# Performance work log

Hardware: AMD Instinct MI355X
Metric: run time of the kernel (lower is better)

## Reference

```python
import jax, jax.numpy as jnp
import numpy as np

EPSILON = 1e-8
DAMPING = 0.7
B, PREV, SIZE, NXT = 8192, 2000, 2000, 2000


def standardize(x):
    # per-sample standardization over features (torch.std uses ddof=1)
    mean = x.mean(axis=1, keepdims=True)
    std = jnp.std(x, axis=1, ddof=1, keepdims=True)
    return (x - mean) / (std + EPSILON)


def setup_inputs() -> dict:
    key = jax.random.key(0)
    ks = jax.random.split(key, 9)
    return {
        "prev_act": jax.random.normal(ks[0], (B, PREV), jnp.float32),
        "self_act": jax.random.normal(ks[1], (B, SIZE), jnp.float32),
        "next_act": jax.random.normal(ks[2], (B, NXT), jnp.float32),
        "forward_W": jax.random.normal(ks[3], (SIZE, PREV), jnp.float32) * 0.02,
        "forward_b": jax.random.normal(ks[4], (SIZE,), jnp.float32) * 0.02,
        "backward_W": jax.random.normal(ks[5], (SIZE, NXT), jnp.float32) * 0.02,
        "backward_b": jax.random.normal(ks[6], (SIZE,), jnp.float32) * 0.02,
        "lateral_W": jax.random.normal(ks[7], (SIZE, SIZE), jnp.float32) * 0.02,
        "lateral_b": jax.random.normal(ks[8], (SIZE,), jnp.float32) * 0.02,
    }


def reference(prev_act, self_act, next_act, forward_W, forward_b,
              backward_W, backward_b, lateral_W, lateral_b):
    # middle HiddenLayer forward: fwd(prev) + next.backward(next) + lateral(self)
    prev_s = standardize(prev_act)   # [B, PREV]
    next_s = standardize(next_act)   # [B, NXT]
    self_s = standardize(self_act)   # [B, SIZE]
    pre = (jnp.einsum('bp,sp->bs', prev_s, forward_W) + forward_b
           + jnp.einsum('bn,sn->bs', next_s, backward_W) + backward_b
           + jnp.einsum('bk,sk->bs', self_s, lateral_W) + lateral_b)
    new_act = jax.nn.relu(pre)
    # damped recurrent update
    return DAMPING * new_act + (1.0 - DAMPING) * self_act
```

## Files before the change

kernel.cpp:

```cpp
#include <hip/hip_runtime.h>
#include <hip/hip_bf16.h>

constexpr int BATCH = 8192;
constexpr int NREAL = 2000;
constexpr int KSLOT = 2048;
constexpr int KPAD  = 6144;
constexpr int NPAD  = 2048;
constexpr int NT    = KPAD / 64;

typedef short bf16x8 __attribute__((ext_vector_type(8)));
typedef float f32x4  __attribute__((ext_vector_type(4)));

__device__ inline void gload_lds16(const void* g, void* l) {
  __builtin_amdgcn_global_load_lds(
      (const __attribute__((address_space(1))) unsigned int*)g,
      (__attribute__((address_space(3))) unsigned int*)l,
      16, 0, 0);
}

__device__ inline unsigned short f2bf(float x) {
  union { float f; unsigned int u; } v;
  v.f = x;
  unsigned int r = v.u + 0x7fffu + ((v.u >> 16) & 1u);
  return (unsigned short)(r >> 16);
}

__global__ __launch_bounds__(256) void pack_kernel(
    const float* __restrict__ prev, const float* __restrict__ nxt,
    const float* __restrict__ selfa,
    const float* __restrict__ fW, const float* __restrict__ bW,
    const float* __restrict__ lW,
    unsigned short* __restrict__ Acat, unsigned short* __restrict__ Wcat) {
  const int mat = blockIdx.y;
  const int t = threadIdx.x;

  if (blockIdx.x >= BATCH) {
    const int s = blockIdx.x - BATCH;
    uint4 q = make_uint4(0, 0, 0, 0);
    if (s < NREAL && t < 250) {
      const float* src = ((mat == 0) ? fW : (mat == 1) ? bW : lW) +
                         (size_t)s * NREAL + t * 8;
      const float4* p = (const float4*)src;
      float4 a = p[0], b = p[1];
      q.x = (unsigned)f2bf(a.x) | ((unsigned)f2bf(a.y) << 16);
      q.y = (unsigned)f2bf(a.z) | ((unsigned)f2bf(a.w) << 16);
      q.z = (unsigned)f2bf(b.x) | ((unsigned)f2bf(b.y) << 16);
      q.w = (unsigned)f2bf(b.z) | ((unsigned)f2bf(b.w) << 16);
    }
    *(uint4*)(Wcat + (size_t)s * KPAD + mat * KSLOT + t * 8) = q;
    return;
  }

  __shared__ float red[4];
  const int row = blockIdx.x;
  const float* src = (mat == 0) ? prev : (mat == 1) ? nxt : selfa;

  float x[8];
  float s1 = 0.f;
  if (t < 250) {
    const float4* p = (const float4*)(src + (size_t)row * NREAL + t * 8);
    float4 a = p[0], b = p[1];
    x[0] = a.x; x[1] = a.y; x[2] = a.z; x[3] = a.w;
    x[4] = b.x; x[5] = b.y; x[6] = b.z; x[7] = b.w;
#pragma unroll
    for (int j = 0; j < 8; ++j) s1 += x[j];
  } else {
#pragma unroll
    for (int j = 0; j < 8; ++j) x[j] = 0.f;
  }
#pragma unroll
  for (int o = 32; o; o >>= 1) s1 += __shfl_xor(s1, o);
  if ((t & 63) == 0) red[t >> 6] = s1;
  __syncthreads();
  const float mean = (red[0] + red[1] + red[2] + red[3]) * (1.f / 2000.f);
  __syncthreads();

  float ss = 0.f;
  if (t < 250) {
#pragma unroll
    for (int j = 0; j < 8; ++j) { float d = x[j] - mean; ss += d * d; }
  }
#pragma unroll
  for (int o = 32; o; o >>= 1) ss += __shfl_xor(ss, o);
  if ((t & 63) == 0) red[t >> 6] = ss;
  __syncthreads();
  const float var = (red[0] + red[1] + red[2] + red[3]) * (1.f / 1999.f);
  const float scale = 1.f / (sqrtf(var) + 1e-8f);

  unsigned short o8[8];
  if (t < 250) {
#pragma unroll
    for (int j = 0; j < 8; ++j) o8[j] = f2bf((x[j] - mean) * scale);
  } else {
#pragma unroll
    for (int j = 0; j < 8; ++j) o8[j] = 0;
  }
  uint4 q;
  q.x = (unsigned)o8[0] | ((unsigned)o8[1] << 16);
  q.y = (unsigned)o8[2] | ((unsigned)o8[3] << 16);
  q.z = (unsigned)o8[4] | ((unsigned)o8[5] << 16);
  q.w = (unsigned)o8[6] | ((unsigned)o8[7] << 16);
  *(uint4*)(Acat + (size_t)row * KPAD + mat * KSLOT + t * 8) = q;
}

__global__ __launch_bounds__(512, 2) void gemm_kernel(
    const unsigned short* __restrict__ A,
    const unsigned short* __restrict__ W,
    const float* __restrict__ fb, const float* __restrict__ bb,
    const float* __restrict__ lb,
    const float* __restrict__ selfact,
    float* __restrict__ out) {
  __shared__ unsigned short lds[2][2][2][256][32];
  unsigned short* ldsF = &lds[0][0][0][0][0];

  const int tid  = threadIdx.x;
  const int wave = tid >> 6;
  const int lane = tid & 63;
  const int wm = wave >> 2;
  const int wn = wave & 3;

  const int nbid = (blockIdx.x & 7) * 32 + (blockIdx.x >> 3);
  const int bm = nbid >> 3;
  const int bn = nbid & 7;

  const int srow = tid >> 2;
  const int sc = (tid & 3) ^ ((srow >> 1) & 3);
  const unsigned short* Asrc =
      A + (size_t)(bm * 256 + srow) * KPAD + sc * 8;
  const unsigned short* Bsrc =
      W + (size_t)(bn * 256 + srow) * KPAD + sc * 8;

  const int pcx = (lane >> 4) ^ ((lane >> 1) & 3);
  const unsigned short* aF = ldsF + (wm * 128 + (lane & 15)) * 32 + pcx * 8;
  const unsigned short* bF = ldsF + (wn * 64 + (lane & 15)) * 32 + pcx * 8;

  f32x4 acc[8][4] = {};
  bf16x8 afA[4], afB[4], bf0[4], bf1[4];

#define STAGE(sb, mat, h, tt) { \
    const unsigned short* g_ = ((mat) ? Bsrc : Asrc) + (size_t)(tt) * 64 + (h) * 32; \
    unsigned short* d_ = ldsF + ((sb) * 4 + (mat) * 2 + (h)) * 8192 + wave * 64 * 8; \
    gload_lds16(g_, d_); \
    gload_lds16(g_ + (size_t)128 * KPAD, d_ + 512 * 8); \
  }

#define READ_AF(dst, bb, kk, mh) \
    _Pragma("unroll") for (int fm = 0; fm < 4; ++fm) \
      dst[fm] = *(const bf16x8*)(aF + ((bb) * 4 + (kk)) * 8192 + ((mh) * 64 + fm * 16) * 32);

#define READ_BF(dst, bb, kk) \
    _Pragma("unroll") for (int fn = 0; fn < 4; ++fn) \
      dst[fn] = *(const bf16x8*)(bF + ((bb) * 4 + 2 + (kk)) * 8192 + (fn * 16) * 32);

#define MFMA16(afr, bfr, mh) { \
    __builtin_amdgcn_s_setprio(1); \
    _Pragma("unroll") for (int fm = 0; fm < 4; ++fm) \
    _Pragma("unroll") for (int fn = 0; fn < 4; ++fn) \
      acc[(mh) * 4 + fm][fn] = __builtin_amdgcn_mfma_f32_16x16x32_bf16( \
          afr[fm], bfr[fn], acc[(mh) * 4 + fm][fn], 0, 0, 0); \
    __builtin_amdgcn_s_setprio(0); \
  }

  STAGE(0, 0, 0, 0)
  STAGE(0, 1, 0, 0)
  STAGE(0, 0, 1, 0)
  STAGE(0, 1, 1, 0)
  asm volatile("s_waitcnt vmcnt(4)" ::: "memory");
  __builtin_amdgcn_s_barrier();
  __builtin_amdgcn_sched_barrier(0);
  READ_AF(afA, 0, 0, 0)
  READ_BF(bf0, 0, 0)

  for (int t = 0; t < NT; ++t) {
    const int b = t & 1;
    const bool pf = (t + 1 < NT);
    __builtin_amdgcn_s_barrier();
    __builtin_amdgcn_sched_barrier(0);
    READ_AF(afB, b, 0, 1)
    if (pf) STAGE(b ^ 1, 0, 0, t + 1)
    MFMA16(afA, bf0, 0)
    asm volatile("s_waitcnt vmcnt(2)" ::: "memory");
    __builtin_amdgcn_s_barrier();
    __builtin_amdgcn_sched_barrier(0);
    READ_AF(afA, b, 1, 0)
    READ_BF(bf1, b, 1)
    if (pf) STAGE(b ^ 1, 1, 0, t + 1)
    MFMA16(afB, bf0, 1)
    __builtin_amdgcn_s_barrier();
    __builtin_amdgcn_sched_barrier(0);
    READ_AF(afB, b, 1, 1)
    if (pf) STAGE(b ^ 1, 0, 1, t + 1)
    MFMA16(afA, bf1, 0)
    asm volatile("s_waitcnt vmcnt(2)" ::: "memory");
    __builtin_amdgcn_s_barrier();
    __builtin_amdgcn_sched_barrier(0);
    if (pf) {
      READ_AF(afA, b ^ 1, 0, 0)
      READ_BF(bf0, b ^ 1, 0)
      STAGE(b ^ 1, 1, 1, t + 1)
    }
    MFMA16(afB, bf1, 1)
  }

  const int colLane = lane & 15;
  const int rowGrp  = (lane >> 4) * 4;
#pragma unroll
  for (int fn = 0; fn < 4; ++fn) {
    const int col = bn * 256 + wn * 64 + fn * 16 + colLane;
    if (col < NREAL) {
      const float bias = fb[col] + bb[col] + lb[col];
#pragma unroll
      for (int m = 0; m < 8; ++m) {
        const int row0 = bm * 256 + wm * 128 + m * 16 + rowGrp;
#pragma unroll
        for (int r = 0; r < 4; ++r) {
          const float pre = acc[m][fn][r] + bias;
          const size_t oi = (size_t)(row0 + r) * NREAL + col;
          out[oi] = 0.7f * fmaxf(pre, 0.f) + 0.3f * selfact[oi];
        }
      }
    }
  }
#undef MFMA16
#undef READ_BF
#undef READ_AF
#undef STAGE
}

extern "C" void kernel_launch(void* const* d_in, const int* in_sizes, int n_in,
                              void* d_out, int out_size, void* d_ws,
                              size_t ws_size, hipStream_t stream) {
  const float* prev = (const float*)d_in[0];
  const float* selfa = (const float*)d_in[1];
  const float* nxt  = (const float*)d_in[2];
  const float* fW = (const float*)d_in[3];
  const float* fb = (const float*)d_in[4];
  const float* bW = (const float*)d_in[5];
  const float* bb = (const float*)d_in[6];
  const float* lW = (const float*)d_in[7];
  const float* lb = (const float*)d_in[8];
  float* out = (float*)d_out;

  unsigned short* Acat = (unsigned short*)d_ws;
  unsigned short* Wcat = Acat + (size_t)BATCH * KPAD;

  pack_kernel<<<dim3(BATCH + NPAD, 3), 256, 0, stream>>>(
      prev, nxt, selfa, fW, bW, lW, Acat, Wcat);
  gemm_kernel<<<dim3(32 * 8), 512, 0, stream>>>(Acat, Wcat, fb, bb, lb,
                                                selfa, out);
}
```

Baseline: 267.5 us.

## Switch GEMM to 128x256 tiles with triple-buffered K=32 LDS pipeline

The GEMM block tile shrinks from 256x256 with 8 waves to 128x256 with 4 waves, and the grid doubles to 512 blocks. The K step drops from 64 to 32 and LDS becomes a three-stage ring, so loads are issued two steps ahead instead of one. The aim is more blocks for occupancy and load balance across CUs, plus deeper latency hiding. In exchange, each A element is reused less, so there is more global traffic per FLOP, more barriers per K, and the schedule is hand-unrolled with hardcoded trip counts.

```diff
diff --git a/kernel.cpp b/kernel.cpp
--- a/kernel.cpp
+++ b/kernel.cpp
@@ -6,7 +6,7 @@
 constexpr int KSLOT = 2048;
 constexpr int KPAD  = 6144;
 constexpr int NPAD  = 2048;
-constexpr int NT    = KPAD / 64;
+constexpr int NT    = KPAD / 32;
 
 typedef short bf16x8 __attribute__((ext_vector_type(8)));
 typedef float f32x4  __attribute__((ext_vector_type(4)));
@@ -103,54 +103,61 @@
   *(uint4*)(Acat + (size_t)row * KPAD + mat * KSLOT + t * 8) = q;
 }
 
-__global__ __launch_bounds__(512, 2) void gemm_kernel(
+__global__ __launch_bounds__(256, 2) void gemm_kernel(
     const unsigned short* __restrict__ A,
     const unsigned short* __restrict__ W,
-    const float* __restrict__ fb, const float* __restrict__ bb,
-    const float* __restrict__ lb,
+    const float* __restrict__ fbv, const float* __restrict__ bbv,
+    const float* __restrict__ lbv,
     const float* __restrict__ selfact,
     float* __restrict__ out) {
-  __shared__ unsigned short lds[2][2][2][256][32];
-  unsigned short* ldsF = &lds[0][0][0][0][0];
+  __shared__ unsigned short lds[3 * 12288];
+  unsigned short* ldsF = lds;
 
   const int tid  = threadIdx.x;
   const int wave = tid >> 6;
   const int lane = tid & 63;
-  const int wm = wave >> 2;
-  const int wn = wave & 3;
-
-  const int nbid = (blockIdx.x & 7) * 32 + (blockIdx.x >> 3);
-  const int bm = nbid >> 3;
-  const int bn = nbid & 7;
+  const int wn = wave;
+
+  const int bn = blockIdx.x & 7;
+  const int bm = blockIdx.x >> 3;
 
   const int srow = tid >> 2;
   const int sc = (tid & 3) ^ ((srow >> 1) & 3);
-  const unsigned short* Asrc =
-      A + (size_t)(bm * 256 + srow) * KPAD + sc * 8;
-  const unsigned short* Bsrc =
-      W + (size_t)(bn * 256 + srow) * KPAD + sc * 8;
+  const unsigned short* Asrc = A + (size_t)(bm * 128 + srow) * KPAD + sc * 8;
+  const unsigned short* Bsrc = W + (size_t)(bn * 256 + srow) * KPAD + sc * 8;
 
   const int pcx = (lane >> 4) ^ ((lane >> 1) & 3);
-  const unsigned short* aF = ldsF + (wm * 128 + (lane & 15)) * 32 + pcx * 8;
-  const unsigned short* bF = ldsF + (wn * 64 + (lane & 15)) * 32 + pcx * 8;
+  const unsigned short* aFb = ldsF + (lane & 15) * 32 + pcx * 8;
+  const unsigned short* bFb = ldsF + 4096 + (wn * 64 + (lane & 15)) * 32 + pcx * 8;
 
   f32x4 acc[8][4] = {};
-  bf16x8 afA[4], afB[4], bf0[4], bf1[4];
-
-#define STAGE(sb, mat, h, tt) { \
-    const unsigned short* g_ = ((mat) ? Bsrc : Asrc) + (size_t)(tt) * 64 + (h) * 32; \
-    unsigned short* d_ = ldsF + ((sb) * 4 + (mat) * 2 + (h)) * 8192 + wave * 64 * 8; \
+  bf16x8 afA[4], afB[4], bf[4];
+
+#define STAGE_A(qq, tt) { \
+    const unsigned short* g_ = Asrc + (size_t)(tt) * 32; \
+    unsigned short* d_ = ldsF + (qq) * 12288 + wave * 512; \
     gload_lds16(g_, d_); \
-    gload_lds16(g_ + (size_t)128 * KPAD, d_ + 512 * 8); \
-  }
-
-#define READ_AF(dst, bb, kk, mh) \
+    gload_lds16(g_ + (size_t)64 * KPAD, d_ + 2048); \
+  }
+#define STAGE_B1(qq, tt) { \
+    const unsigned short* g_ = Bsrc + (size_t)(tt) * 32; \
+    unsigned short* d_ = ldsF + (qq) * 12288 + 4096 + wave * 512; \
+    gload_lds16(g_, d_); \
+  }
+#define STAGE_B2(qq, tt) { \
+    const unsigned short* g_ = Bsrc + (size_t)(tt) * 32 + (size_t)64 * KPAD; \
+    unsigned short* d_ = ldsF + (qq) * 12288 + 4096 + 2048 + wave * 512; \
+    gload_lds16(g_, d_); \
+    gload_lds16(g_ + (size_t)64 * KPAD, d_ + 2048); \
+    gload_lds16(g_ + (size_t)128 * KPAD, d_ + 4096); \
+  }
+
+#define READ_AF(dst, qq, mh) \
     _Pragma("unroll") for (int fm = 0; fm < 4; ++fm) \
-      dst[fm] = *(const bf16x8*)(aF + ((bb) * 4 + (kk)) * 8192 + ((mh) * 64 + fm * 16) * 32);
-
-#define READ_BF(dst, bb, kk) \
+      dst[fm] = *(const bf16x8*)(aFb + (qq) * 12288 + ((mh) * 4 + fm) * 512);
+#define READ_BF(dst, qq) \
     _Pragma("unroll") for (int fn = 0; fn < 4; ++fn) \
-      dst[fn] = *(const bf16x8*)(bF + ((bb) * 4 + 2 + (kk)) * 8192 + (fn * 16) * 32);
+      dst[fn] = *(const bf16x8*)(bFb + (qq) * 12288 + fn * 512);
 
 #define MFMA16(afr, bfr, mh) { \
     __builtin_amdgcn_s_setprio(1); \
@@ -161,46 +168,39 @@
     __builtin_amdgcn_s_setprio(0); \
   }
 
-  STAGE(0, 0, 0, 0)
-  STAGE(0, 1, 0, 0)
-  STAGE(0, 0, 1, 0)
-  STAGE(0, 1, 1, 0)
-  asm volatile("s_waitcnt vmcnt(4)" ::: "memory");
+#define PH1(q, t, DS) { \
+    __builtin_amdgcn_s_barrier(); \
+    __builtin_amdgcn_sched_barrier(0); \
+    READ_BF(bf, q) \
+    READ_AF(afB, q, 1) \
+    if (DS) { STAGE_A((((q) + 2) % 3), (t) + 2) STAGE_B1((((q) + 2) % 3), (t) + 2) } \
+    MFMA16(afA, bf, 0) \
+  }
+#define PH2(q, t, VM, DS, RN) { \
+    asm volatile("s_waitcnt vmcnt(" VM ")" ::: "memory"); \
+    __builtin_amdgcn_s_barrier(); \
+    __builtin_amdgcn_sched_barrier(0); \
+    if (RN) { READ_AF(afA, (((q) + 1) % 3), 0) } \
+    if (DS) { STAGE_B2((((q) + 2) % 3), (t) + 2) } \
+    MFMA16(afB, bf, 1) \
+  }
+
+  STAGE_A(0, 0) STAGE_B1(0, 0) STAGE_B2(0, 0)
+  STAGE_A(1, 1) STAGE_B1(1, 1) STAGE_B2(1, 1)
+  asm volatile("s_waitcnt vmcnt(6)" ::: "memory");
   __builtin_amdgcn_s_barrier();
   __builtin_amdgcn_sched_barrier(0);
-  READ_AF(afA, 0, 0, 0)
-  READ_BF(bf0, 0, 0)
-
-  for (int t = 0; t < NT; ++t) {
-    const int b = t & 1;
-    const bool pf = (t + 1 < NT);
-    __builtin_amdgcn_s_barrier();
-    __builtin_amdgcn_sched_barrier(0);
-    READ_AF(afB, b, 0, 1)
-    if (pf) STAGE(b ^ 1, 0, 0, t + 1)
-    MFMA16(afA, bf0, 0)
-    asm volatile("s_waitcnt vmcnt(2)" ::: "memory");
-    __builtin_amdgcn_s_barrier();
-    __builtin_amdgcn_sched_barrier(0);
-    READ_AF(afA, b, 1, 0)
-    READ_BF(bf1, b, 1)
-    if (pf) STAGE(b ^ 1, 1, 0, t + 1)
-    MFMA16(afB, bf0, 1)
-    __builtin_amdgcn_s_barrier();
-    __builtin_amdgcn_sched_barrier(0);
-    READ_AF(afB, b, 1, 1)
-    if (pf) STAGE(b ^ 1, 0, 1, t + 1)
-    MFMA16(afA, bf1, 0)
-    asm volatile("s_waitcnt vmcnt(2)" ::: "memory");
-    __builtin_amdgcn_s_barrier();
-    __builtin_amdgcn_sched_barrier(0);
-    if (pf) {
-      READ_AF(afA, b ^ 1, 0, 0)
-      READ_BF(bf0, b ^ 1, 0)
-      STAGE(b ^ 1, 1, 1, t + 1)
-    }
-    MFMA16(afB, bf1, 1)
-  }
+  READ_AF(afA, 0, 0)
+
+  for (int i = 0; i < 63; ++i) {
+    const int t = i * 3;
+    PH1(0, t, true)     PH2(0, t, "3", true, true)
+    PH1(1, t + 1, true) PH2(1, t + 1, "3", true, true)
+    PH1(2, t + 2, true) PH2(2, t + 2, "3", true, true)
+  }
+  PH1(0, 189, true)  PH2(0, 189, "3", true, true)
+  PH1(1, 190, false) PH2(1, 190, "0", false, true)
+  PH1(2, 191, false) PH2(2, 191, "0", false, false)
 
   const int colLane = lane & 15;
   const int rowGrp  = (lane >> 4) * 4;
@@ -208,10 +208,10 @@
   for (int fn = 0; fn < 4; ++fn) {
     const int col = bn * 256 + wn * 64 + fn * 16 + colLane;
     if (col < NREAL) {
-      const float bias = fb[col] + bb[col] + lb[col];
+      const float bias = fbv[col] + bbv[col] + lbv[col];
 #pragma unroll
       for (int m = 0; m < 8; ++m) {
-        const int row0 = bm * 256 + wm * 128 + m * 16 + rowGrp;
+        const int row0 = bm * 128 + m * 16 + rowGrp;
 #pragma unroll
         for (int r = 0; r < 4; ++r) {
           const float pre = acc[m][fn][r] + bias;
@@ -221,10 +221,14 @@
       }
     }
   }
+#undef PH2
+#undef PH1
 #undef MFMA16
 #undef READ_BF
 #undef READ_AF
-#undef STAGE
+#undef STAGE_B2
+#undef STAGE_B1
+#undef STAGE_A
 }
 
 extern "C" void kernel_launch(void* const* d_in, const int* in_sizes, int n_in,
@@ -246,6 +250,6 @@
 
   pack_kernel<<<dim3(BATCH + NPAD, 3), 256, 0, stream>>>(
       prev, nxt, selfa, fW, bW, lW, Acat, Wcat);
-  gemm_kernel<<<dim3(32 * 8), 512, 0, stream>>>(Acat, Wcat, fb, bb, lb,
+  gemm_kernel<<<dim3(64 * 8), 256, 0, stream>>>(Acat, Wcat, fb, bb, lb,
                                                 selfa, out);
 }
```

New measurement: 280.8 us. 5.0% more time.

## Use 4-wave GEMM blocks with 128x128 per-wave tiles and deeper prefetch

Applied to the files above, without the earlier changes.

The GEMM block shrinks from 8 waves to 4. Each wave now computes a 128x128 output tile with 64 accumulators, which doubles register reuse of the A and B fragments per LDS read. The pipeline is reorganised into two phases per K-tile and prefetches half-tiles two steps ahead, with explicit vmcnt waits and a peeled epilogue. The price is heavy register pressure from 256 accumulator VGPRs plus fragments, and fewer waves per CU to hide latency.

```diff
diff --git a/kernel.cpp b/kernel.cpp
--- a/kernel.cpp
+++ b/kernel.cpp
@@ -103,7 +103,7 @@
   *(uint4*)(Acat + (size_t)row * KPAD + mat * KSLOT + t * 8) = q;
 }
 
-__global__ __launch_bounds__(512, 2) void gemm_kernel(
+__global__ __launch_bounds__(256, 1) void gemm_kernel(
     const unsigned short* __restrict__ A,
     const unsigned short* __restrict__ W,
     const float* __restrict__ fb, const float* __restrict__ bb,
@@ -116,15 +116,15 @@
   const int tid  = threadIdx.x;
   const int wave = tid >> 6;
   const int lane = tid & 63;
-  const int wm = wave >> 2;
-  const int wn = wave & 3;
+  const int wm = wave >> 1;
+  const int wn = wave & 1;
 
   const int nbid = (blockIdx.x & 7) * 32 + (blockIdx.x >> 3);
   const int bm = nbid >> 3;
   const int bn = nbid & 7;
 
   const int srow = tid >> 2;
-  const int sc = (tid & 3) ^ ((srow >> 1) & 3);
+  const int sc = (tid & 3) ^ ((tid >> 3) & 3);
   const unsigned short* Asrc =
       A + (size_t)(bm * 256 + srow) * KPAD + sc * 8;
   const unsigned short* Bsrc =
@@ -132,99 +132,102 @@
 
   const int pcx = (lane >> 4) ^ ((lane >> 1) & 3);
   const unsigned short* aF = ldsF + (wm * 128 + (lane & 15)) * 32 + pcx * 8;
-  const unsigned short* bF = ldsF + (wn * 64 + (lane & 15)) * 32 + pcx * 8;
-
-  f32x4 acc[8][4] = {};
-  bf16x8 afA[4], afB[4], bf0[4], bf1[4];
-
-#define STAGE(sb, mat, h, tt) { \
-    const unsigned short* g_ = ((mat) ? Bsrc : Asrc) + (size_t)(tt) * 64 + (h) * 32; \
-    unsigned short* d_ = ldsF + ((sb) * 4 + (mat) * 2 + (h)) * 8192 + wave * 64 * 8; \
-    gload_lds16(g_, d_); \
-    gload_lds16(g_ + (size_t)128 * KPAD, d_ + 512 * 8); \
-  }
-
-#define READ_AF(dst, bb, kk, mh) \
-    _Pragma("unroll") for (int fm = 0; fm < 4; ++fm) \
-      dst[fm] = *(const bf16x8*)(aF + ((bb) * 4 + (kk)) * 8192 + ((mh) * 64 + fm * 16) * 32);
-
-#define READ_BF(dst, bb, kk) \
-    _Pragma("unroll") for (int fn = 0; fn < 4; ++fn) \
-      dst[fn] = *(const bf16x8*)(bF + ((bb) * 4 + 2 + (kk)) * 8192 + (fn * 16) * 32);
-
-#define MFMA16(afr, bfr, mh) { \
-    __builtin_amdgcn_s_setprio(1); \
-    _Pragma("unroll") for (int fm = 0; fm < 4; ++fm) \
-    _Pragma("unroll") for (int fn = 0; fn < 4; ++fn) \
-      acc[(mh) * 4 + fm][fn] = __builtin_amdgcn_mfma_f32_16x16x32_bf16( \
-          afr[fm], bfr[fn], acc[(mh) * 4 + fm][fn], 0, 0, 0); \
-    __builtin_amdgcn_s_setprio(0); \
-  }
-
-  STAGE(0, 0, 0, 0)
-  STAGE(0, 1, 0, 0)
-  STAGE(0, 0, 1, 0)
-  STAGE(0, 1, 1, 0)
-  asm volatile("s_waitcnt vmcnt(4)" ::: "memory");
+  const unsigned short* bF = ldsF + (wn * 128 + (lane & 15)) * 32 + pcx * 8;
+
+  f32x4 acc[8][8] = {};
+  bf16x8 afA[8], afB[8], bfr[8];
+
+#define STAGE_H(sb, h, tt) { \
+    const unsigned short* gA_ = Asrc + (size_t)(tt) * 64 + (h) * 32; \
+    const unsigned short* gB_ = Bsrc + (size_t)(tt) * 64 + (h) * 32; \
+    unsigned short* dA_ = ldsF + ((sb) * 4 + (h)) * 8192 + wave * 512; \
+    unsigned short* dB_ = ldsF + ((sb) * 4 + 2 + (h)) * 8192 + wave * 512; \
+    gload_lds16(gA_, dA_); \
+    gload_lds16(gA_ + (size_t)64 * KPAD, dA_ + 2048); \
+    gload_lds16(gA_ + (size_t)128 * KPAD, dA_ + 4096); \
+    gload_lds16(gA_ + (size_t)192 * KPAD, dA_ + 6144); \
+    gload_lds16(gB_, dB_); \
+    gload_lds16(gB_ + (size_t)64 * KPAD, dB_ + 2048); \
+    gload_lds16(gB_ + (size_t)128 * KPAD, dB_ + 4096); \
+    gload_lds16(gB_ + (size_t)192 * KPAD, dB_ + 6144); \
+  }
+
+#define READ_BF(b, kk) \
+    _Pragma("unroll") for (int fn = 0; fn < 8; ++fn) \
+      bfr[fn] = *(const bf16x8*)(bF + ((b) * 4 + 2 + (kk)) * 8192 + fn * 512);
+
+#define READ_AF(dst, b, kk) \
+    _Pragma("unroll") for (int fm = 0; fm < 8; ++fm) \
+      dst[fm] = *(const bf16x8*)(aF + ((b) * 4 + (kk)) * 8192 + fm * 512);
+
+#define MFMA64(afr) \
+    _Pragma("unroll") for (int fn = 0; fn < 8; ++fn) \
+    _Pragma("unroll") for (int fm = 0; fm < 8; ++fm) \
+      acc[fm][fn] = __builtin_amdgcn_mfma_f32_16x16x32_bf16( \
+          afr[fm], bfr[fn], acc[fm][fn], 0, 0, 0);
+
+#define PHA(b, t, DS, VM) { \
+    asm volatile("s_waitcnt vmcnt(" VM ")" ::: "memory"); \
+    __builtin_amdgcn_s_barrier(); \
+    __builtin_amdgcn_sched_barrier(0); \
+    READ_BF(b, 0) \
+    READ_AF(afB, b, 1) \
+    if (DS) STAGE_H((b) ^ 1, 1, (t) + 1) \
+    MFMA64(afA) \
+  }
+#define PHB(b, t, DS, RA, VM) { \
+    asm volatile("s_waitcnt vmcnt(" VM ")" ::: "memory"); \
+    __builtin_amdgcn_s_barrier(); \
+    __builtin_amdgcn_sched_barrier(0); \
+    READ_BF(b, 1) \
+    if (RA) READ_AF(afA, (b) ^ 1, 0) \
+    if (DS) STAGE_H(b, 0, (t) + 2) \
+    MFMA64(afB) \
+  }
+
+  STAGE_H(0, 0, 0)
+  STAGE_H(0, 1, 0)
+  STAGE_H(1, 0, 1)
+  asm volatile("s_waitcnt vmcnt(16)" ::: "memory");
   __builtin_amdgcn_s_barrier();
   __builtin_amdgcn_sched_barrier(0);
-  READ_AF(afA, 0, 0, 0)
-  READ_BF(bf0, 0, 0)
-
-  for (int t = 0; t < NT; ++t) {
+  READ_AF(afA, 0, 0)
+
+  for (int t = 0; t < NT - 2; ++t) {
     const int b = t & 1;
-    const bool pf = (t + 1 < NT);
-    __builtin_amdgcn_s_barrier();
-    __builtin_amdgcn_sched_barrier(0);
-    READ_AF(afB, b, 0, 1)
-    if (pf) STAGE(b ^ 1, 0, 0, t + 1)
-    MFMA16(afA, bf0, 0)
-    asm volatile("s_waitcnt vmcnt(2)" ::: "memory");
-    __builtin_amdgcn_s_barrier();
-    __builtin_amdgcn_sched_barrier(0);
-    READ_AF(afA, b, 1, 0)
-    READ_BF(bf1, b, 1)
-    if (pf) STAGE(b ^ 1, 1, 0, t + 1)
-    MFMA16(afB, bf0, 1)
-    __builtin_amdgcn_s_barrier();
-    __builtin_amdgcn_sched_barrier(0);
-    READ_AF(afB, b, 1, 1)
-    if (pf) STAGE(b ^ 1, 0, 1, t + 1)
-    MFMA16(afA, bf1, 0)
-    asm volatile("s_waitcnt vmcnt(2)" ::: "memory");
-    __builtin_amdgcn_s_barrier();
-    __builtin_amdgcn_sched_barrier(0);
-    if (pf) {
-      READ_AF(afA, b ^ 1, 0, 0)
-      READ_BF(bf0, b ^ 1, 0)
-      STAGE(b ^ 1, 1, 1, t + 1)
-    }
-    MFMA16(afB, bf1, 1)
-  }
+    PHA(b, t, true, "8")
+    PHB(b, t, true, true, "8")
+  }
+  PHA(0, NT - 2, true, "8")
+  PHB(0, NT - 2, false, true, "8")
+  PHA(1, NT - 1, false, "0")
+  PHB(1, NT - 1, false, false, "0")
 
   const int colLane = lane & 15;
   const int rowGrp  = (lane >> 4) * 4;
 #pragma unroll
-  for (int fn = 0; fn < 4; ++fn) {
-    const int col = bn * 256 + wn * 64 + fn * 16 + colLane;
+  for (int fn = 0; fn < 8; ++fn) {
+    const int col = bn * 256 + wn * 128 + fn * 16 + colLane;
     if (col < NREAL) {
       const float bias = fb[col] + bb[col] + lb[col];
 #pragma unroll
-      for (int m = 0; m < 8; ++m) {
-        const int row0 = bm * 256 + wm * 128 + m * 16 + rowGrp;
+      for (int fm = 0; fm < 8; ++fm) {
+        const int row0 = bm * 256 + wm * 128 + fm * 16 + rowGrp;
 #pragma unroll
         for (int r = 0; r < 4; ++r) {
-          const float pre = acc[m][fn][r] + bias;
+          const float pre = acc[fm][fn][r] + bias;
           const size_t oi = (size_t)(row0 + r) * NREAL + col;
           out[oi] = 0.7f * fmaxf(pre, 0.f) + 0.3f * selfact[oi];
         }
       }
     }
   }
-#undef MFMA16
+#undef PHB
+#undef PHA
+#undef MFMA64
+#undef READ_AF
 #undef READ_BF
-#undef READ_AF
-#undef STAGE
+#undef STAGE_H
 }
 
 extern "C" void kernel_launch(void* const* d_in, const int* in_sizes, int n_in,
@@ -246,6 +249,6 @@
 
   pack_kernel<<<dim3(BATCH + NPAD, 3), 256, 0, stream>>>(
       prev, nxt, selfa, fW, bW, lW, Acat, Wcat);
-  gemm_kernel<<<dim3(32 * 8), 512, 0, stream>>>(Acat, Wcat, fb, bb, lb,
+  gemm_kernel<<<dim3(32 * 8), 256, 0, stream>>>(Acat, Wcat, fb, bb, lb,
                                                 selfa, out);
 }
```

After: 296.6 us. 1.11x slower.

## Restructure GEMM pipeline with triple-buffered A, double-buffered B, and XOR swizzle

Applied to the files above, without the earlier changes.

Replaces the two-half double-buffered LDS staging with a unified 160KB LDS buffer. A tiles are triple-buffered and B tiles double-buffered, with a full 64-wide K tile per stage and an XOR row-swizzle to avoid bank conflicts. Each iteration now issues two 32-MFMA phases with only one barrier instead of four smaller phases with four barriers, prefetching A two tiles ahead. This is meant to cut synchronisation overhead and hide global latency better. The cost is much higher LDS use, which likely limits occupancy to one block per CU despite launch_bounds(512,2), plus more live fragment registers.

```diff
diff --git a/kernel.cpp b/kernel.cpp
--- a/kernel.cpp
+++ b/kernel.cpp
@@ -110,8 +110,7 @@
     const float* __restrict__ lb,
     const float* __restrict__ selfact,
     float* __restrict__ out) {
-  __shared__ unsigned short lds[2][2][2][256][32];
-  unsigned short* ldsF = &lds[0][0][0][0][0];
+  __shared__ unsigned short ldsS[81920];
 
   const int tid  = threadIdx.x;
   const int wave = tid >> 6;
@@ -123,83 +122,84 @@
   const int bm = nbid >> 3;
   const int bn = nbid & 7;
 
-  const int srow = tid >> 2;
-  const int sc = (tid & 3) ^ ((srow >> 1) & 3);
-  const unsigned short* Asrc =
-      A + (size_t)(bm * 256 + srow) * KPAD + sc * 8;
-  const unsigned short* Bsrc =
-      W + (size_t)(bn * 256 + srow) * KPAD + sc * 8;
-
-  const int pcx = (lane >> 4) ^ ((lane >> 1) & 3);
-  const unsigned short* aF = ldsF + (wm * 128 + (lane & 15)) * 32 + pcx * 8;
-  const unsigned short* bF = ldsF + (wn * 64 + (lane & 15)) * 32 + pcx * 8;
+  const unsigned short* Ap[4];
+  const unsigned short* Bp[4];
+#pragma unroll
+  for (int c = 0; c < 4; ++c) {
+    const int p = c * 512 + tid;
+    const int srow = p >> 3;
+    const int cph = p & 7;
+    const int key = (srow ^ (srow >> 3)) & 7;
+    const int clog = cph ^ key;
+    Ap[c] = A + (size_t)(bm * 256 + srow) * KPAD + clog * 8;
+    Bp[c] = W + (size_t)(bn * 256 + srow) * KPAD + clog * 8;
+  }
+
+  int offAs[8], offBs[4];
+#pragma unroll
+  for (int fm = 0; fm < 8; ++fm) {
+    const int row = wm * 128 + fm * 16 + (lane & 15);
+    const int key = (row ^ (row >> 3)) & 7;
+    offAs[fm] = (row * 128 + (((lane >> 4) ^ key) << 4)) >> 1;
+  }
+#pragma unroll
+  for (int fn = 0; fn < 4; ++fn) {
+    const int row = wn * 64 + fn * 16 + (lane & 15);
+    const int key = (row ^ (row >> 3)) & 7;
+    offBs[fn] = (row * 128 + (((lane >> 4) ^ key) << 4)) >> 1;
+  }
 
   f32x4 acc[8][4] = {};
-  bf16x8 afA[4], afB[4], bf0[4], bf1[4];
-
-#define STAGE(sb, mat, h, tt) { \
-    const unsigned short* g_ = ((mat) ? Bsrc : Asrc) + (size_t)(tt) * 64 + (h) * 32; \
-    unsigned short* d_ = ldsF + ((sb) * 4 + (mat) * 2 + (h)) * 8192 + wave * 64 * 8; \
-    gload_lds16(g_, d_); \
-    gload_lds16(g_ + (size_t)128 * KPAD, d_ + 512 * 8); \
-  }
-
-#define READ_AF(dst, bb, kk, mh) \
-    _Pragma("unroll") for (int fm = 0; fm < 4; ++fm) \
-      dst[fm] = *(const bf16x8*)(aF + ((bb) * 4 + (kk)) * 8192 + ((mh) * 64 + fm * 16) * 32);
-
-#define READ_BF(dst, bb, kk) \
+  bf16x8 afr[8], bfr[4];
+
+#define STAGE_A(qq, tt) { \
+    _Pragma("unroll") for (int c = 0; c < 4; ++c) \
+      gload_lds16(Ap[c] + (size_t)(tt) * 64, \
+                  &ldsS[(qq) * 16384 + c * 4096 + wave * 512]); }
+#define STAGE_B(rr, tt) { \
+    _Pragma("unroll") for (int c = 0; c < 4; ++c) \
+      gload_lds16(Bp[c] + (size_t)(tt) * 64, \
+                  &ldsS[49152 + (rr) * 16384 + c * 4096 + wave * 512]); }
+
+#define READ_PH(qq, rr, kk) \
+    _Pragma("unroll") for (int fm = 0; fm < 8; ++fm) \
+      afr[fm] = *(const bf16x8*)&ldsS[(qq) * 16384 + (offAs[fm] ^ ((kk) << 5))]; \
     _Pragma("unroll") for (int fn = 0; fn < 4; ++fn) \
-      dst[fn] = *(const bf16x8*)(bF + ((bb) * 4 + 2 + (kk)) * 8192 + (fn * 16) * 32);
-
-#define MFMA16(afr, bfr, mh) { \
+      bfr[fn] = *(const bf16x8*)&ldsS[49152 + (rr) * 16384 + (offBs[fn] ^ ((kk) << 5))];
+
+#define MFMA32 { \
     __builtin_amdgcn_s_setprio(1); \
-    _Pragma("unroll") for (int fm = 0; fm < 4; ++fm) \
+    _Pragma("unroll") for (int fm = 0; fm < 8; ++fm) \
     _Pragma("unroll") for (int fn = 0; fn < 4; ++fn) \
-      acc[(mh) * 4 + fm][fn] = __builtin_amdgcn_mfma_f32_16x16x32_bf16( \
-          afr[fm], bfr[fn], acc[(mh) * 4 + fm][fn], 0, 0, 0); \
+      acc[fm][fn] = __builtin_amdgcn_mfma_f32_16x16x32_bf16( \
+          afr[fm], bfr[fn], acc[fm][fn], 0, 0, 0); \
     __builtin_amdgcn_s_setprio(0); \
   }
 
-  STAGE(0, 0, 0, 0)
-  STAGE(0, 1, 0, 0)
-  STAGE(0, 0, 1, 0)
-  STAGE(0, 1, 1, 0)
-  asm volatile("s_waitcnt vmcnt(4)" ::: "memory");
+  STAGE_A(0, 0)
+  STAGE_B(0, 0)
+  STAGE_A(1, 1)
+  STAGE_B(1, 1)
+  asm volatile("s_waitcnt vmcnt(8)" ::: "memory");
   __builtin_amdgcn_s_barrier();
   __builtin_amdgcn_sched_barrier(0);
-  READ_AF(afA, 0, 0, 0)
-  READ_BF(bf0, 0, 0)
 
   for (int t = 0; t < NT; ++t) {
-    const int b = t & 1;
-    const bool pf = (t + 1 < NT);
+    const int q = t % 3;
+    const int r = t & 1;
+    READ_PH(q, r, 0)
+    if (t >= 1 && t + 1 < NT) STAGE_B(r ^ 1, t + 1)
+    MFMA32
+    READ_PH(q, r, 1)
+    if (t + 2 < NT) STAGE_A((t + 2) % 3, t + 2)
+    MFMA32
+    if (t < NT - 2) {
+      asm volatile("s_waitcnt vmcnt(4)" ::: "memory");
+    } else {
+      asm volatile("s_waitcnt vmcnt(0)" ::: "memory");
+    }
     __builtin_amdgcn_s_barrier();
     __builtin_amdgcn_sched_barrier(0);
-    READ_AF(afB, b, 0, 1)
-    if (pf) STAGE(b ^ 1, 0, 0, t + 1)
-    MFMA16(afA, bf0, 0)
-    asm volatile("s_waitcnt vmcnt(2)" ::: "memory");
-    __builtin_amdgcn_s_barrier();
-    __builtin_amdgcn_sched_barrier(0);
-    READ_AF(afA, b, 1, 0)
-    READ_BF(bf1, b, 1)
-    if (pf) STAGE(b ^ 1, 1, 0, t + 1)
-    MFMA16(afB, bf0, 1)
-    __builtin_amdgcn_s_barrier();
-    __builtin_amdgcn_sched_barrier(0);
-    READ_AF(afB, b, 1, 1)
-    if (pf) STAGE(b ^ 1, 0, 1, t + 1)
-    MFMA16(afA, bf1, 0)
-    asm volatile("s_waitcnt vmcnt(2)" ::: "memory");
-    __builtin_amdgcn_s_barrier();
-    __builtin_amdgcn_sched_barrier(0);
-    if (pf) {
-      READ_AF(afA, b ^ 1, 0, 0)
-      READ_BF(bf0, b ^ 1, 0)
-      STAGE(b ^ 1, 1, 1, t + 1)
-    }
-    MFMA16(afB, bf1, 1)
   }
 
   const int colLane = lane & 15;
@@ -210,21 +210,21 @@
     if (col < NREAL) {
       const float bias = fb[col] + bb[col] + lb[col];
 #pragma unroll
-      for (int m = 0; m < 8; ++m) {
-        const int row0 = bm * 256 + wm * 128 + m * 16 + rowGrp;
-#pragma unroll
-        for (int r = 0; r < 4; ++r) {
-          const float pre = acc[m][fn][r] + bias;
-          const size_t oi = (size_t)(row0 + r) * NREAL + col;
+      for (int fm = 0; fm < 8; ++fm) {
+        const int row0 = bm * 256 + wm * 128 + fm * 16 + rowGrp;
+#pragma unroll
+        for (int rr = 0; rr < 4; ++rr) {
+          const float pre = acc[fm][fn][rr] + bias;
+          const size_t oi = (size_t)(row0 + rr) * NREAL + col;
           out[oi] = 0.7f * fmaxf(pre, 0.f) + 0.3f * selfact[oi];
         }
       }
     }
   }
-#undef MFMA16
-#undef READ_BF
-#undef READ_AF
-#undef STAGE
+#undef MFMA32
+#undef READ_PH
+#undef STAGE_B
+#undef STAGE_A
 }
 
 extern "C" void kernel_launch(void* const* d_in, const int* in_sizes, int n_in,
```

Result: no change. 262.6 us (-1.8%).
